# Kernel tuning notes

Measured on AMD Instinct MI355X. Metric: run time of the kernel, lower is better.

The kernel has to match this reference:

```python
import jax, jax.numpy as jnp
import numpy as np

B, T, C = 4, 2048, 1024
N_HEADS = 16
HEAD_DIM = C // N_HEADS


def setup_inputs() -> dict:
    key = jax.random.key(0)
    k1, k2, k3 = jax.random.split(key, 3)
    x = jax.random.normal(k1, (B, T, C), dtype=jnp.float32)
    # torch Linear weights stored as [out, in]; we store as [in, out] for x @ W
    w_qkv = jax.random.normal(k2, (C, 3 * C), dtype=jnp.float32) * (1.0 / np.sqrt(C))
    w_proj = jax.random.normal(k3, (C, C), dtype=jnp.float32) * (1.0 / np.sqrt(C))
    return {"x": x, "w_qkv": w_qkv, "w_proj": w_proj}


def reference(x, w_qkv, w_proj):
    Bx, Tx, Cx = x.shape
    qkv = x @ w_qkv                               # [B,T,3C]
    q, k, v = jnp.split(qkv, 3, axis=-1)

    def to_heads(t):
        return t.reshape(Bx, Tx, N_HEADS, HEAD_DIM).transpose(0, 2, 1, 3)  # [B,H,T,D]

    q, k, v = to_heads(q), to_heads(k), to_heads(v)
    scale = 1.0 / np.sqrt(HEAD_DIM).astype(np.float32)
    scores = jnp.einsum('bhqd,bhkd->bhqk', q, k) * scale  # [B,H,T,T]
    causal = jnp.tril(jnp.ones((Tx, Tx), dtype=bool))
    scores = jnp.where(causal[None, None, :, :], scores, -jnp.inf)
    weights = jax.nn.softmax(scores, axis=-1)
    out = jnp.einsum('bhqk,bhkd->bhqd', weights, v)       # [B,H,T,D]
    out = out.transpose(0, 2, 1, 3).reshape(Bx, Tx, Cx)   # [B,T,C]
    return out @ w_proj
```

## Files before the change

### kernel.cpp

```cpp
#include <hip/hip_runtime.h>
#include <hip/hip_bf16.h>

typedef unsigned short u16;
typedef unsigned int u32;
typedef __attribute__((ext_vector_type(8))) __bf16 bf16x8;
typedef __attribute__((ext_vector_type(4))) float f32x4;
typedef __attribute__((ext_vector_type(4))) short short4v;
typedef __attribute__((ext_vector_type(2))) u32 u32x2;

#define B_ 4
#define T_ 2048
#define C_ 1024
#define NH_ 16
#define HD_ 64

static __device__ __forceinline__ u16 f2bf(float f) {
  u32 u = __builtin_bit_cast(u32, f);
  u32 r = (u + 0x7fffu + ((u >> 16) & 1u)) >> 16;
  return (u16)r;
}

static __device__ __forceinline__ u32 pack2bf(float a, float b) {
  u32 ua = __builtin_bit_cast(u32, a) + 0x8000u;
  u32 ub = __builtin_bit_cast(u32, b) + 0x8000u;
  return __builtin_amdgcn_perm(ub, ua, 0x07060302u);
}

static __device__ __forceinline__ float fexp2(float x) {
#if __has_builtin(__builtin_amdgcn_exp2f)
  return __builtin_amdgcn_exp2f(x);
#else
  return exp2f(x);
#endif
}

static __device__ __forceinline__ void load_lds16(const u16* g, u16* l) {
  __builtin_amdgcn_global_load_lds(
      (const __attribute__((address_space(1))) u32*)g,
      (__attribute__((address_space(3))) u32*)l, 16, 0, 0);
}

static __device__ __forceinline__ f32x4 mfma32(bf16x8 a, bf16x8 b, f32x4 c) {
  return __builtin_amdgcn_mfma_f32_16x16x32_bf16(a, b, c, 0, 0, 0);
}

static __device__ __forceinline__ f32x4 mfma16(short4v a, short4v b, f32x4 c) {
#if __has_builtin(__builtin_amdgcn_mfma_f32_16x16x16bf16_1k)
  return __builtin_amdgcn_mfma_f32_16x16x16bf16_1k(a, b, c, 0, 0, 0);
#else
  asm volatile("v_mfma_f32_16x16x16_bf16 %0, %1, %2, %0\n\t"
               "s_nop 7\n\ts_nop 7"
               : "+v"(c)
               : "v"(a), "v"(b));
  return c;
#endif
}

__global__ __launch_bounds__(256) void cast_bf(const float* __restrict__ in,
                                               u16* __restrict__ out, int n) {
  int i = (blockIdx.x * 256 + threadIdx.x) * 8;
  if (i >= n) return;
  float4 a = *(const float4*)(in + i);
  float4 b = *(const float4*)(in + i + 4);
  u16 r[8] = {f2bf(a.x), f2bf(a.y), f2bf(a.z), f2bf(a.w),
              f2bf(b.x), f2bf(b.y), f2bf(b.z), f2bf(b.w)};
  *(uint4*)(out + i) = *(const uint4*)r;
}

__global__ __launch_bounds__(256) void transpose_cast(const float* __restrict__ in,
                                                      u16* __restrict__ out,
                                                      int K, int N) {
  __shared__ float tile[32][33];
  int bx = blockIdx.x * 32;
  int by = blockIdx.y * 32;
  int tx = threadIdx.x & 31, ty = threadIdx.x >> 5;
  for (int r = ty; r < 32; r += 8)
    tile[r][tx] = in[(size_t)(by + r) * N + bx + tx];
  __syncthreads();
  for (int r = ty; r < 32; r += 8)
    out[(size_t)(bx + r) * K + by + tx] = f2bf(tile[tx][r]);
}

template <bool STORE_BF16>
__global__ __launch_bounds__(256) void gemm_bt(const u16* __restrict__ A,
                                               const u16* __restrict__ Bt,
                                               void* __restrict__ Cv,
                                               int M, int N, int K) {
  __shared__ __align__(16) u16 As[128 * 64];
  __shared__ __align__(16) u16 Bs[128 * 64];
  const int tid = threadIdx.x;
  const int wave = tid >> 6, lane = tid & 63;
  const int wm = (wave >> 1) * 64, wn = (wave & 1) * 64;
  const int m0 = blockIdx.x * 128, n0 = blockIdx.y * 128;
  const int col = lane & 15, quad = lane >> 4;
  const int kq = quad << 3;
  const int lrow = lane >> 3, lcol = (lane & 7) * 8;

  f32x4 acc[4][4] = {};

  for (int kt = 0; kt < K; kt += 64) {
    __syncthreads();
    for (int i = 0; i < 4; i++) {
      int row = (wave * 4 + i) * 8 + lrow;
      load_lds16(A + (size_t)(m0 + row) * K + kt + lcol, &As[row * 64 + lcol]);
      load_lds16(Bt + (size_t)(n0 + row) * K + kt + lcol, &Bs[row * 64 + lcol]);
    }
    __syncthreads();
    for (int ks = 0; ks < 64; ks += 32) {
      bf16x8 af[4], bfr[4];
      for (int t = 0; t < 4; t++) {
        af[t]  = *(const bf16x8*)(&As[(wm + t * 16 + col) * 64 + ks + kq]);
        bfr[t] = *(const bf16x8*)(&Bs[(wn + t * 16 + col) * 64 + ks + kq]);
      }
      for (int i = 0; i < 4; i++)
        for (int j = 0; j < 4; j++)
          acc[i][j] = mfma32(af[i], bfr[j], acc[i][j]);
    }
  }

  const int rbase = quad * 4;
  for (int i = 0; i < 4; i++)
    for (int j = 0; j < 4; j++) {
      int r = m0 + wm + i * 16 + rbase;
      int c = n0 + wn + j * 16 + col;
      if (STORE_BF16) {
        for (int reg = 0; reg < 4; reg++)
          ((u16*)Cv)[(size_t)(r + reg) * N + c] = f2bf(acc[i][j][reg]);
      } else {
        for (int reg = 0; reg < 4; reg++)
          ((float*)Cv)[(size_t)(r + reg) * N + c] = acc[i][j][reg];
      }
    }
}

__global__ __launch_bounds__(256) void v_permute(const u16* __restrict__ qkv,
                                                 u16* __restrict__ vt) {
  const int jt = blockIdx.x, bh = blockIdx.y, b = bh >> 4, h = bh & 15;
  __shared__ u16 tile[64][68];
  const int tid = threadIdx.x;
  {
    int tl = tid >> 2, c = (tid & 3) * 16;
    const u16* src = qkv + (size_t)(b * 2048 + jt * 64 + tl) * 3072 + 2048 + h * 64 + c;
    *(uint4*)(&tile[tl][c])     = *(const uint4*)(src);
    *(uint4*)(&tile[tl][c + 8]) = *(const uint4*)(src + 8);
  }
  __syncthreads();
  int d = tid >> 2, gq = tid & 3;
  u16 ob[16] __attribute__((aligned(16)));
  for (int j = 0; j < 16; j++) {
    int g = gq * 16 + j;
    int tl = (g & 3) | (((g >> 4) & 3) << 2) | (((g >> 2) & 3) << 4);
    ob[j] = tile[tl][d];
  }
  u16* dst = vt + ((size_t)bh * 64 + d) * 2048 + jt * 64 + gq * 16;
  *(uint4*)(dst) = *(const uint4*)ob;
  *(uint4*)(dst + 8) = *(const uint4*)(ob + 8);
}

__global__ __launch_bounds__(256, 2) void attn_fused(const u16* __restrict__ qkv,
                                                     const u16* __restrict__ vt,
                                                     u16* __restrict__ o) {
  const int i = blockIdx.x >> 6;
  const int bh = blockIdx.x & 63, b = bh >> 4, h = bh & 15;
  const int tid = threadIdx.x, wave = tid >> 6, lane = tid & 63;
  const int col = lane & 15, quad = lane >> 4;

  const int qtv[4] = {2 * i, 2 * i + 1, 30 - 2 * i, 31 - 2 * i};
  const int jtmax = 31 - 2 * i;

  __shared__ __align__(16) u16 Ks[2][4096];
  __shared__ __align__(16) u16 Vs[2][4096];

  const u16* qkb = qkv + (size_t)b * 2048 * 3072;
  const u16* vtb = vt + (size_t)bh * 64 * 2048;

  bf16x8 qf[4][2];
  for (int t = 0; t < 4; t++) {
    int q = qtv[t] * 64 + wave * 16 + col;
    const u16* qp = qkb + (size_t)q * 3072 + h * 64;
    qf[t][0] = *(const bf16x8*)(qp + quad * 8);
    qf[t][1] = *(const bf16x8*)(qp + 32 + quad * 8);
  }

  float m_i[4] = {-INFINITY, -INFINITY, -INFINITY, -INFINITY};
  float l_i[4] = {0.f, 0.f, 0.f, 0.f};
  f32x4 Oacc[4][4] = {};

  const float scale2 = 0.125f * 1.44269504f;

  auto stage = [&](int jt, int buf) {
    for (int ii = 0; ii < 2; ii++) {
      int idx = (ii * 4 + wave) * 64 + lane;
      int r = idx >> 3, c = (idx & 7) * 8;
      load_lds16(qkb + (size_t)(jt * 64 + r) * 3072 + 1024 + h * 64 + c,
                 &Ks[buf][idx * 8]);
      load_lds16(vtb + (size_t)r * 2048 + jt * 64 + c, &Vs[buf][idx * 8]);
    }
  };

  auto softmax_tile = [&](f32x4* s, int t, u32* pbt) {
    float mx = s[0][0];
    for (int nt = 0; nt < 4; nt++)
      for (int r = 0; r < 4; r++) mx = fmaxf(mx, s[nt][r]);
    mx = fmaxf(mx, __shfl_xor(mx, 16, 64));
    mx = fmaxf(mx, __shfl_xor(mx, 32, 64));
    float mn = fmaxf(m_i[t], mx);
    float alpha = fexp2(m_i[t] - mn);
    float psum = 0.f;
    for (int nt = 0; nt < 4; nt++)
      for (int r = 0; r < 4; r++) {
        float p = fexp2(s[nt][r] - mn);
        s[nt][r] = p;
        psum += p;
      }
    psum += __shfl_xor(psum, 16, 64);
    psum += __shfl_xor(psum, 32, 64);
    l_i[t] = l_i[t] * alpha + psum;
    m_i[t] = mn;
    for (int nt = 0; nt < 4; nt++) {
      pbt[nt * 2]     = pack2bf(s[nt][0], s[nt][1]);
      pbt[nt * 2 + 1] = pack2bf(s[nt][2], s[nt][3]);
    }
    for (int dt = 0; dt < 4; dt++)
      for (int r = 0; r < 4; r++) Oacc[t][dt][r] *= alpha;
  };

  stage(0, 0);
  for (int jt = 0; jt <= jtmax; jt++) {
    const int cur = jt & 1;
    __syncthreads();
    if (jt < jtmax) stage(jt + 1, cur ^ 1);

    const u16* K_ = Ks[cur];
    const u16* V_ = Vs[cur];
    bool act[4];
    for (int t = 0; t < 4; t++) act[t] = (jt <= qtv[t]);

    u32 pb[4][8];
    for (int pr = 0; pr < 2; pr++) {
      const int t0 = pr * 2, t1 = pr * 2 + 1;
      if (!act[t1]) continue;
      f32x4 s0[4] = {}, s1[4] = {};
      for (int nt = 0; nt < 4; nt++) {
        bf16x8 k0 = *(const bf16x8*)(K_ + (nt * 16 + col) * 64 + quad * 8);
        bf16x8 k1 = *(const bf16x8*)(K_ + (nt * 16 + col) * 64 + 32 + quad * 8);
        if (act[t0]) {
          s0[nt] = mfma32(k0, qf[t0][0], s0[nt]);
          s0[nt] = mfma32(k1, qf[t0][1], s0[nt]);
        }
        s1[nt] = mfma32(k0, qf[t1][0], s1[nt]);
        s1[nt] = mfma32(k1, qf[t1][1], s1[nt]);
      }
      if (act[t0]) {
        if (jt == qtv[t0]) {
          for (int nt = 0; nt < 4; nt++)
            for (int r = 0; r < 4; r++) {
              int j = nt * 16 + quad * 4 + r, q = wave * 16 + col;
              s0[nt][r] = (j > q) ? -INFINITY : s0[nt][r] * scale2;
            }
        } else {
          for (int nt = 0; nt < 4; nt++)
            for (int r = 0; r < 4; r++) s0[nt][r] *= scale2;
        }
        softmax_tile(s0, t0, pb[t0]);
      }
      if (jt == qtv[t1]) {
        for (int nt = 0; nt < 4; nt++)
          for (int r = 0; r < 4; r++) {
            int j = nt * 16 + quad * 4 + r, q = wave * 16 + col;
            s1[nt][r] = (j > q) ? -INFINITY : s1[nt][r] * scale2;
          }
      } else {
        for (int nt = 0; nt < 4; nt++)
          for (int r = 0; r < 4; r++) s1[nt][r] *= scale2;
      }
      softmax_tile(s1, t1, pb[t1]);
    }

    for (int dt = 0; dt < 4; dt++) {
      uint4 vb0 = *(const uint4*)(V_ + (dt * 16 + col) * 64 + quad * 16);
      uint4 vb1 = *(const uint4*)(V_ + (dt * 16 + col) * 64 + quad * 16 + 8);
      short4v vf[4];
      vf[0] = __builtin_bit_cast(short4v, (u32x2){vb0.x, vb0.y});
      vf[1] = __builtin_bit_cast(short4v, (u32x2){vb0.z, vb0.w});
      vf[2] = __builtin_bit_cast(short4v, (u32x2){vb1.x, vb1.y});
      vf[3] = __builtin_bit_cast(short4v, (u32x2){vb1.z, vb1.w});
      for (int t = 0; t < 4; t++) {
        if (!act[t]) continue;
        for (int nt = 0; nt < 4; nt++) {
          short4v pf = __builtin_bit_cast(
              short4v, (u32x2){pb[t][nt * 2], pb[t][nt * 2 + 1]});
          Oacc[t][dt] = mfma16(vf[nt], pf, Oacc[t][dt]);
        }
      }
    }
  }

  for (int t = 0; t < 4; t++) {
    float rl = 1.0f / l_i[t];
    int q = qtv[t] * 64 + wave * 16 + col;
    u16* op = o + (size_t)(b * 2048 + q) * 1024 + h * 64;
    for (int dt = 0; dt < 4; dt++) {
      u16 ob[4] __attribute__((aligned(8)));
      for (int r = 0; r < 4; r++) ob[r] = f2bf(Oacc[t][dt][r] * rl);
      *(uint2*)(op + dt * 16 + quad * 4) = *(const uint2*)ob;
    }
  }
}

extern "C" void kernel_launch(void* const* d_in, const int* in_sizes, int n_in,
                              void* d_out, int out_size, void* d_ws, size_t ws_size,
                              hipStream_t stream) {
  const float* x      = (const float*)d_in[0];
  const float* w_qkv  = (const float*)d_in[1];
  const float* w_proj = (const float*)d_in[2];
  float* out = (float*)d_out;

  u16* x_bf    = (u16*)d_ws;
  u16* wqkvT   = x_bf + (size_t)8192 * 1024;
  u16* wprojT  = wqkvT + (size_t)3072 * 1024;
  u16* qkv_bf  = wprojT + (size_t)1024 * 1024;
  u16* attn_bf = qkv_bf + (size_t)8192 * 3072;
  u16* vt_perm = x_bf;

  cast_bf<<<4096, 256, 0, stream>>>(x, x_bf, 8192 * 1024);
  transpose_cast<<<dim3(96, 32), 256, 0, stream>>>(w_qkv, wqkvT, 1024, 3072);
  transpose_cast<<<dim3(32, 32), 256, 0, stream>>>(w_proj, wprojT, 1024, 1024);

  gemm_bt<true><<<dim3(64, 24), 256, 0, stream>>>(x_bf, wqkvT, qkv_bf, 8192, 3072, 1024);

  v_permute<<<dim3(32, 64), 256, 0, stream>>>(qkv_bf, vt_perm);

  attn_fused<<<512, 256, 0, stream>>>(qkv_bf, vt_perm, attn_bf);

  gemm_bt<false><<<dim3(64, 8), 256, 0, stream>>>(attn_bf, wprojT, out, 8192, 1024, 1024);
}
```

Before: 290.3 us.

## Swizzle LDS tiles, fold softmax scale into QKV GEMM, halve attention block work

Applies an XOR swizzle to the LDS layout of the GEMM A/B tiles and the attention K/V tiles to cut bank conflicts on the fragment reads. Folds the softmax scale times log2(e) into the Q columns of the QKV GEMM epilogue, so the attention loop no longer multiplies the scores. Each attention block now handles two query tiles instead of four (grid doubled to 1024, launch bounds set to 4 blocks per SM) to reduce register pressure and raise occupancy. Q is now rounded to bf16 after scaling, which slightly changes the rounding behaviour.

Result: faster. 271.3 us (-6.5%).

```diff
diff --git a/kernel.cpp b/kernel.cpp
--- a/kernel.cpp
+++ b/kernel.cpp
@@ -81,11 +81,12 @@
     out[(size_t)(bx + r) * K + by + tx] = f2bf(tile[tx][r]);
 }
 
-template <bool STORE_BF16>
+template <bool STORE_BF16, bool SCALE_Q>
 __global__ __launch_bounds__(256) void gemm_bt(const u16* __restrict__ A,
                                                const u16* __restrict__ Bt,
                                                void* __restrict__ Cv,
-                                               int M, int N, int K) {
+                                               int M, int N, int K,
+                                               float qscale) {
   __shared__ __align__(16) u16 As[128 * 64];
   __shared__ __align__(16) u16 Bs[128 * 64];
   const int tid = threadIdx.x;
@@ -93,24 +94,26 @@
   const int wm = (wave >> 1) * 64, wn = (wave & 1) * 64;
   const int m0 = blockIdx.x * 128, n0 = blockIdx.y * 128;
   const int col = lane & 15, quad = lane >> 4;
-  const int kq = quad << 3;
-  const int lrow = lane >> 3, lcol = (lane & 7) * 8;
+  const int lcol = (lane & 7) * 8;
+  const int sg = ((lane & 7) ^ ((lane >> 3) & 7)) * 8;
+  const int ag = ((quad ^ (col & 7)) * 8);
 
   f32x4 acc[4][4] = {};
 
   for (int kt = 0; kt < K; kt += 64) {
     __syncthreads();
     for (int i = 0; i < 4; i++) {
-      int row = (wave * 4 + i) * 8 + lrow;
-      load_lds16(A + (size_t)(m0 + row) * K + kt + lcol, &As[row * 64 + lcol]);
-      load_lds16(Bt + (size_t)(n0 + row) * K + kt + lcol, &Bs[row * 64 + lcol]);
+      int row = (wave * 4 + i) * 8 + (lane >> 3);
+      load_lds16(A + (size_t)(m0 + row) * K + kt + sg, &As[row * 64 + lcol]);
+      load_lds16(Bt + (size_t)(n0 + row) * K + kt + sg, &Bs[row * 64 + lcol]);
     }
     __syncthreads();
     for (int ks = 0; ks < 64; ks += 32) {
+      const int o = ag ^ ks;
       bf16x8 af[4], bfr[4];
       for (int t = 0; t < 4; t++) {
-        af[t]  = *(const bf16x8*)(&As[(wm + t * 16 + col) * 64 + ks + kq]);
-        bfr[t] = *(const bf16x8*)(&Bs[(wn + t * 16 + col) * 64 + ks + kq]);
+        af[t]  = *(const bf16x8*)(&As[(wm + t * 16 + col) * 64 + o]);
+        bfr[t] = *(const bf16x8*)(&Bs[(wn + t * 16 + col) * 64 + o]);
       }
       for (int i = 0; i < 4; i++)
         for (int j = 0; j < 4; j++)
@@ -123,9 +126,10 @@
     for (int j = 0; j < 4; j++) {
       int r = m0 + wm + i * 16 + rbase;
       int c = n0 + wn + j * 16 + col;
+      float sc = (SCALE_Q && c < 1024) ? qscale : 1.0f;
       if (STORE_BF16) {
         for (int reg = 0; reg < 4; reg++)
-          ((u16*)Cv)[(size_t)(r + reg) * N + c] = f2bf(acc[i][j][reg]);
+          ((u16*)Cv)[(size_t)(r + reg) * N + c] = f2bf(acc[i][j][reg] * sc);
       } else {
         for (int reg = 0; reg < 4; reg++)
           ((float*)Cv)[(size_t)(r + reg) * N + c] = acc[i][j][reg];
@@ -157,7 +161,7 @@
   *(uint4*)(dst + 8) = *(const uint4*)(ob + 8);
 }
 
-__global__ __launch_bounds__(256, 2) void attn_fused(const u16* __restrict__ qkv,
+__global__ __launch_bounds__(256, 4) void attn_fused(const u16* __restrict__ qkv,
                                                      const u16* __restrict__ vt,
                                                      u16* __restrict__ o) {
   const int i = blockIdx.x >> 6;
@@ -165,8 +169,8 @@
   const int tid = threadIdx.x, wave = tid >> 6, lane = tid & 63;
   const int col = lane & 15, quad = lane >> 4;
 
-  const int qtv[4] = {2 * i, 2 * i + 1, 30 - 2 * i, 31 - 2 * i};
-  const int jtmax = 31 - 2 * i;
+  const int qt0 = i, qt1 = 31 - i;
+  const int jtmax = qt1;
 
   __shared__ __align__(16) u16 Ks[2][4096];
   __shared__ __align__(16) u16 Vs[2][4096];
@@ -174,27 +178,30 @@
   const u16* qkb = qkv + (size_t)b * 2048 * 3072;
   const u16* vtb = vt + (size_t)bh * 64 * 2048;
 
-  bf16x8 qf[4][2];
-  for (int t = 0; t < 4; t++) {
-    int q = qtv[t] * 64 + wave * 16 + col;
+  bf16x8 qf[2][2];
+  for (int t = 0; t < 2; t++) {
+    int q = (t ? qt1 : qt0) * 64 + wave * 16 + col;
     const u16* qp = qkb + (size_t)q * 3072 + h * 64;
     qf[t][0] = *(const bf16x8*)(qp + quad * 8);
     qf[t][1] = *(const bf16x8*)(qp + 32 + quad * 8);
   }
 
-  float m_i[4] = {-INFINITY, -INFINITY, -INFINITY, -INFINITY};
-  float l_i[4] = {0.f, 0.f, 0.f, 0.f};
-  f32x4 Oacc[4][4] = {};
-
-  const float scale2 = 0.125f * 1.44269504f;
+  float m_i[2] = {-INFINITY, -INFINITY};
+  float l_i[2] = {0.f, 0.f};
+  f32x4 Oacc[2][4] = {};
+
+  const int sg  = ((lane & 7) ^ ((lane >> 3) & 7)) * 8;
+  const int swq = col & 7;
+  const int kg0 = (quad ^ swq) * 8;
+  const int vg0 = ((2 * quad) ^ swq) * 8;
 
   auto stage = [&](int jt, int buf) {
     for (int ii = 0; ii < 2; ii++) {
       int idx = (ii * 4 + wave) * 64 + lane;
-      int r = idx >> 3, c = (idx & 7) * 8;
-      load_lds16(qkb + (size_t)(jt * 64 + r) * 3072 + 1024 + h * 64 + c,
+      int r = idx >> 3;
+      load_lds16(qkb + (size_t)(jt * 64 + r) * 3072 + 1024 + h * 64 + sg,
                  &Ks[buf][idx * 8]);
-      load_lds16(vtb + (size_t)r * 2048 + jt * 64 + c, &Vs[buf][idx * 8]);
+      load_lds16(vtb + (size_t)r * 2048 + jt * 64 + sg, &Vs[buf][idx * 8]);
     }
   };
 
@@ -233,72 +240,62 @@
 
     const u16* K_ = Ks[cur];
     const u16* V_ = Vs[cur];
-    bool act[4];
-    for (int t = 0; t < 4; t++) act[t] = (jt <= qtv[t]);
-
-    u32 pb[4][8];
-    for (int pr = 0; pr < 2; pr++) {
-      const int t0 = pr * 2, t1 = pr * 2 + 1;
-      if (!act[t1]) continue;
-      f32x4 s0[4] = {}, s1[4] = {};
-      for (int nt = 0; nt < 4; nt++) {
-        bf16x8 k0 = *(const bf16x8*)(K_ + (nt * 16 + col) * 64 + quad * 8);
-        bf16x8 k1 = *(const bf16x8*)(K_ + (nt * 16 + col) * 64 + 32 + quad * 8);
-        if (act[t0]) {
-          s0[nt] = mfma32(k0, qf[t0][0], s0[nt]);
-          s0[nt] = mfma32(k1, qf[t0][1], s0[nt]);
-        }
-        s1[nt] = mfma32(k0, qf[t1][0], s1[nt]);
-        s1[nt] = mfma32(k1, qf[t1][1], s1[nt]);
-      }
-      if (act[t0]) {
-        if (jt == qtv[t0]) {
-          for (int nt = 0; nt < 4; nt++)
-            for (int r = 0; r < 4; r++) {
-              int j = nt * 16 + quad * 4 + r, q = wave * 16 + col;
-              s0[nt][r] = (j > q) ? -INFINITY : s0[nt][r] * scale2;
-            }
-        } else {
-          for (int nt = 0; nt < 4; nt++)
-            for (int r = 0; r < 4; r++) s0[nt][r] *= scale2;
-        }
-        softmax_tile(s0, t0, pb[t0]);
-      }
-      if (jt == qtv[t1]) {
+    const bool act0 = (jt <= qt0);
+
+    f32x4 s0[4] = {}, s1[4] = {};
+    for (int nt = 0; nt < 4; nt++) {
+      bf16x8 k0 = *(const bf16x8*)(K_ + (nt * 16 + col) * 64 + kg0);
+      bf16x8 k1 = *(const bf16x8*)(K_ + (nt * 16 + col) * 64 + (kg0 ^ 32));
+      if (act0) {
+        s0[nt] = mfma32(k0, qf[0][0], s0[nt]);
+        s0[nt] = mfma32(k1, qf[0][1], s0[nt]);
+      }
+      s1[nt] = mfma32(k0, qf[1][0], s1[nt]);
+      s1[nt] = mfma32(k1, qf[1][1], s1[nt]);
+    }
+
+    u32 pb0[8], pb1[8];
+    if (act0) {
+      if (jt == qt0) {
         for (int nt = 0; nt < 4; nt++)
           for (int r = 0; r < 4; r++) {
             int j = nt * 16 + quad * 4 + r, q = wave * 16 + col;
-            s1[nt][r] = (j > q) ? -INFINITY : s1[nt][r] * scale2;
+            if (j > q) s0[nt][r] = -INFINITY;
           }
-      } else {
-        for (int nt = 0; nt < 4; nt++)
-          for (int r = 0; r < 4; r++) s1[nt][r] *= scale2;
-      }
-      softmax_tile(s1, t1, pb[t1]);
-    }
+      }
+      softmax_tile(s0, 0, pb0);
+    }
+    if (jt == qt1) {
+      for (int nt = 0; nt < 4; nt++)
+        for (int r = 0; r < 4; r++) {
+          int j = nt * 16 + quad * 4 + r, q = wave * 16 + col;
+          if (j > q) s1[nt][r] = -INFINITY;
+        }
+    }
+    softmax_tile(s1, 1, pb1);
 
     for (int dt = 0; dt < 4; dt++) {
-      uint4 vb0 = *(const uint4*)(V_ + (dt * 16 + col) * 64 + quad * 16);
-      uint4 vb1 = *(const uint4*)(V_ + (dt * 16 + col) * 64 + quad * 16 + 8);
+      uint4 vb0 = *(const uint4*)(V_ + (dt * 16 + col) * 64 + vg0);
+      uint4 vb1 = *(const uint4*)(V_ + (dt * 16 + col) * 64 + (vg0 ^ 8));
       short4v vf[4];
       vf[0] = __builtin_bit_cast(short4v, (u32x2){vb0.x, vb0.y});
       vf[1] = __builtin_bit_cast(short4v, (u32x2){vb0.z, vb0.w});
       vf[2] = __builtin_bit_cast(short4v, (u32x2){vb1.x, vb1.y});
       vf[3] = __builtin_bit_cast(short4v, (u32x2){vb1.z, vb1.w});
-      for (int t = 0; t < 4; t++) {
-        if (!act[t]) continue;
-        for (int nt = 0; nt < 4; nt++) {
-          short4v pf = __builtin_bit_cast(
-              short4v, (u32x2){pb[t][nt * 2], pb[t][nt * 2 + 1]});
-          Oacc[t][dt] = mfma16(vf[nt], pf, Oacc[t][dt]);
+      for (int nt = 0; nt < 4; nt++) {
+        if (act0) {
+          short4v pf0 = __builtin_bit_cast(short4v, (u32x2){pb0[nt * 2], pb0[nt * 2 + 1]});
+          Oacc[0][dt] = mfma16(vf[nt], pf0, Oacc[0][dt]);
         }
-      }
-    }
-  }
-
-  for (int t = 0; t < 4; t++) {
+        short4v pf1 = __builtin_bit_cast(short4v, (u32x2){pb1[nt * 2], pb1[nt * 2 + 1]});
+        Oacc[1][dt] = mfma16(vf[nt], pf1, Oacc[1][dt]);
+      }
+    }
+  }
+
+  for (int t = 0; t < 2; t++) {
     float rl = 1.0f / l_i[t];
-    int q = qtv[t] * 64 + wave * 16 + col;
+    int q = (t ? qt1 : qt0) * 64 + wave * 16 + col;
     u16* op = o + (size_t)(b * 2048 + q) * 1024 + h * 64;
     for (int dt = 0; dt < 4; dt++) {
       u16 ob[4] __attribute__((aligned(8)));
@@ -323,15 +320,19 @@
   u16* attn_bf = qkv_bf + (size_t)8192 * 3072;
   u16* vt_perm = x_bf;
 
+  const float qscale = 0.125f * 1.44269504f;
+
   cast_bf<<<4096, 256, 0, stream>>>(x, x_bf, 8192 * 1024);
   transpose_cast<<<dim3(96, 32), 256, 0, stream>>>(w_qkv, wqkvT, 1024, 3072);
   transpose_cast<<<dim3(32, 32), 256, 0, stream>>>(w_proj, wprojT, 1024, 1024);
 
-  gemm_bt<true><<<dim3(64, 24), 256, 0, stream>>>(x_bf, wqkvT, qkv_bf, 8192, 3072, 1024);
+  gemm_bt<true, true><<<dim3(64, 24), 256, 0, stream>>>(
+      x_bf, wqkvT, qkv_bf, 8192, 3072, 1024, qscale);
 
   v_permute<<<dim3(32, 64), 256, 0, stream>>>(qkv_bf, vt_perm);
 
-  attn_fused<<<512, 256, 0, stream>>>(qkv_bf, vt_perm, attn_bf);
-
-  gemm_bt<false><<<dim3(64, 8), 256, 0, stream>>>(attn_bf, wprojT, out, 8192, 1024, 1024);
-}
+  attn_fused<<<1024, 256, 0, stream>>>(qkv_bf, vt_perm, attn_bf);
+
+  gemm_bt<false, false><<<dim3(64, 8), 256, 0, stream>>>(
+      attn_bf, wprojT, out, 8192, 1024, 1024, 1.0f);
+}
```
